# Kernel tuning notes

Hardware: AMD Instinct MI355X
Metric: run time of the kernel (lower is better)

The kernel has to match this reference:

```python
import jax, jax.numpy as jnp
import numpy as np

# Module dims (match init_kwargs): c_in=1, khop=3, f=128, c_out=2, f_out=128
N, KHOP, NNB, C_IN, F_IN = 2048, 3, 16, 1, 128
C_OUT, F_OUT = 2, 128
EPS_ROOT, EPS_NORM = 1e-8, 1e-7


def setup_inputs() -> dict:
    key = jax.random.key(0)
    k1, k2, k3 = jax.random.split(key, 3)
    x = jax.random.normal(k1, (N, C_IN, F_IN), jnp.float32)
    # dense form of the ragged neighbor[i][k] -> (n, c, f) lists
    neighbor = jax.random.normal(k2, (N, KHOP, NNB, C_IN, F_IN), jnp.float32)
    # Conv1d(khop*c_in, c_out*f_out, kernel_size=f, bias=False) weight
    W = jax.random.normal(k3, (C_OUT * F_OUT, KHOP * C_IN, F_IN), jnp.float32) * 0.05
    return {"x": x, "neighbor": neighbor, "W": W}


def _sgnroot(a):
    return jnp.sign(a) * jnp.sqrt(jnp.clip(jnp.abs(a), EPS_ROOT))


def _row_normalize(a):
    a = a / (jnp.abs(a).sum(-2, keepdims=True) + EPS_NORM)
    return jnp.where(jnp.isnan(a), 0.0, a)


def _feature_adjacency(x, neighbor):
    # x: (N,c,f), neighbor: (N,k,n,c,f) -> fadj: (N,k,f,f)
    fadj = jnp.einsum('Nca,Nkncb->Nkab', x, neighbor)
    fadj = fadj + jnp.swapaxes(fadj, -1, -2)
    return _row_normalize(_sgnroot(fadj))


def _transform(z, adj, W):
    # z: (..., c, f); adj: (..., K, f, f) broadcastable against z's batch dims
    # y[..., K, c, a] = sum_b adj[..., K, a, b] * z[..., c, b]
    y = jnp.einsum('...kab,...cb->...kca', adj, z)
    y = y.reshape(y.shape[:-3] + (KHOP * C_IN, F_IN))  # (..., k*c, f)
    # Conv1d with kernel_size == f and output length 1 == full contraction
    out = jnp.einsum('oqf,...qf->...o', W, y)
    return out.reshape(out.shape[:-1] + (C_OUT, F_OUT))


def reference(x, neighbor, W):
    adj = _feature_adjacency(x, neighbor)                     # (N,k,f,f)
    x_out = _transform(x, adj, W)                             # (N,c_out,f_out)
    # each neighbor[i,k] is transformed with the full per-sample adj[i]
    nbr_out = _transform(neighbor, adj[:, None, None], W)     # (N,k,n,c_out,f_out)
    return (x_out, nbr_out)
```

## Files before the change

kernel.cpp:

```cpp
#include <hip/hip_runtime.h>

typedef unsigned short u16;
typedef unsigned int u32;
typedef __bf16 bf16;
typedef __bf16 bf16x8 __attribute__((ext_vector_type(8)));
typedef __bf16 bf16x4 __attribute__((ext_vector_type(4)));
typedef float f32x4 __attribute__((ext_vector_type(4)));

#define NSAMP 2048
#define KH 3
#define NNBR 16
#define F 128
#define OUT_O 256
#define QT 384

#define ZLD 136
#define YLD 136

__device__ __forceinline__ bf16x4 cvt4(float4 v) {
    bf16x4 h;
    h[0] = (bf16)v.x; h[1] = (bf16)v.y; h[2] = (bf16)v.z; h[3] = (bf16)v.w;
    return h;
}

__global__ void wprep(const float* __restrict__ W, bf16* __restrict__ Wbf) {
    int i = blockIdx.x * 256 + threadIdx.x;
    if (i < OUT_O * QT) Wbf[i] = (bf16)W[i];
}

__launch_bounds__(512, 6)
__global__ void featkhop(const float* __restrict__ xg,
                         const float* __restrict__ ng,
                         const bf16* __restrict__ Wbf,
                         float* __restrict__ out) {
    __shared__ __align__(16) bf16 Zs[64 * ZLD];
    __shared__ __align__(16) bf16 Ys[2][64 * YLD];
    float* const xls = (float*)(Zs + 49 * ZLD);
    float* const sls = xls + F;
    float* const rsi = xls + 4 * F;

    const int i = blockIdx.x;
    const int t = threadIdx.x;
    const int lane = t & 63;
    const int w = t >> 6;
    const int lr = lane & 15;
    const int lg = lane >> 4;

    if (t < F / 4) {
        float4 v = *(const float4*)(xg + (size_t)i * F + t * 4);
        *(float4*)(xls + t * 4) = v;
        *(bf16x4*)(Zs + 0 * ZLD + t * 4) = cvt4(v);
    }
    const float* nb = ng + (size_t)i * (KH * NNBR * F);
    {
        #pragma unroll
        for (int c = 0; c < 3; ++c) {
            int j = c * 512 + t;
            float4 v = *(const float4*)(nb + j * 4);
            int fl = j * 4;
            int row = 1 + (fl >> 7);
            int b = fl & 127;
            *(bf16x4*)(Zs + row * ZLD + b) = cvt4(v);
        }
    }
    if (t < KH * F) {
        int q = t >> 7, b = t & 127;
        float s = 0.f;
        #pragma unroll
        for (int n = 0; n < NNBR; ++n) s += nb[(q * NNBR + n) * F + b];
        sls[q * F + b] = s;
    }
    __syncthreads();

    const int a_row = w * 16 + lr;
    const float x_a = xls[a_row];
    const int cbase = lg * 8;

    f32x4 acc2[4][2];
    {
        f32x4 zf = {0.f, 0.f, 0.f, 0.f};
        #pragma unroll
        for (int mt = 0; mt < 4; ++mt) { acc2[mt][0] = zf; acc2[mt][1] = zf; }
    }

    for (int q = 0; q < KH; ++q) {
        const float s_a = sls[q * F + a_row];
        bf16x8 uvh[4];
        float ps = 0.f;
        #pragma unroll
        for (int kk = 0; kk < 4; ++kk) {
            float4 xb0 = *(const float4*)(xls + kk * 32 + cbase);
            float4 xb1 = *(const float4*)(xls + kk * 32 + cbase + 4);
            float4 sb0 = *(const float4*)(sls + q * F + kk * 32 + cbase);
            float4 sb1 = *(const float4*)(sls + q * F + kk * 32 + cbase + 4);
            float xb[8] = {xb0.x, xb0.y, xb0.z, xb0.w, xb1.x, xb1.y, xb1.z, xb1.w};
            float sb[8] = {sb0.x, sb0.y, sb0.z, sb0.w, sb1.x, sb1.y, sb1.z, sb1.w};
            #pragma unroll
            for (int e = 0; e < 8; ++e) {
                float tv = x_a * sb[e] + xb[e] * s_a;
                float r = tv * __builtin_amdgcn_rsqf(fmaxf(fabsf(tv), 1e-8f));
                uvh[kk][e] = (bf16)r;
                ps += fabsf(r);
            }
        }
        ps += __shfl_xor(ps, 16);
        ps += __shfl_xor(ps, 32);
        if (lg == 0) rsi[a_row] = __builtin_amdgcn_rcpf(ps + 1e-7f);
        __syncthreads();

        bf16x8 afrag[4];
        #pragma unroll
        for (int kk = 0; kk < 4; ++kk) {
            float4 r0 = *(const float4*)(rsi + kk * 32 + cbase);
            float4 r1 = *(const float4*)(rsi + kk * 32 + cbase + 4);
            float rb[8] = {r0.x, r0.y, r0.z, r0.w, r1.x, r1.y, r1.z, r1.w};
            #pragma unroll
            for (int e = 0; e < 8; ++e)
                afrag[kk][e] = (bf16)((float)uvh[kk][e] * rb[e]);
        }

        bf16* Ysb = Ys[q & 1];
        #pragma unroll
        for (int mt = 0; mt < 4; ++mt) {
            f32x4 a1 = {0.f, 0.f, 0.f, 0.f};
            #pragma unroll
            for (int kk = 0; kk < 4; ++kk) {
                bf16x8 zfrag = *(const bf16x8*)(Zs + (mt * 16 + lr) * ZLD + kk * 32 + cbase);
                a1 = __builtin_amdgcn_mfma_f32_16x16x32_bf16(afrag[kk], zfrag, a1, 0, 0, 0);
            }
            bf16x4 yv;
            #pragma unroll
            for (int r = 0; r < 4; ++r) yv[r] = (bf16)a1[r];
            *(bf16x4*)(Ysb + (mt * 16 + lr) * YLD + w * 16 + lg * 4) = yv;
        }
        __syncthreads();

        #pragma unroll
        for (int kk = 0; kk < 4; ++kk) {
            const bf16* wp = Wbf + (size_t)(w * 32 + lr) * QT + q * F + kk * 32 + cbase;
            bf16x8 wf0 = *(const bf16x8*)wp;
            bf16x8 wf1 = *(const bf16x8*)(wp + 16 * QT);
            #pragma unroll
            for (int mt = 0; mt < 4; ++mt) {
                bf16x8 af = *(const bf16x8*)(Ysb + (mt * 16 + lr) * YLD + kk * 32 + cbase);
                acc2[mt][0] = __builtin_amdgcn_mfma_f32_16x16x32_bf16(af, wf0, acc2[mt][0], 0, 0, 0);
                acc2[mt][1] = __builtin_amdgcn_mfma_f32_16x16x32_bf16(af, wf1, acc2[mt][1], 0, 0, 0);
            }
        }
    }

    float* xout = out + (size_t)i * OUT_O;
    float* nout = out + (size_t)NSAMP * OUT_O + (size_t)i * 48 * OUT_O;
    #pragma unroll
    for (int mt = 0; mt < 4; ++mt) {
        #pragma unroll
        for (int r = 0; r < 4; ++r) {
            int v = mt * 16 + lg * 4 + r;
            #pragma unroll
            for (int nn = 0; nn < 2; ++nn) {
                int o = w * 32 + nn * 16 + lr;
                float val = acc2[mt][nn][r];
                if (v == 0) xout[o] = val;
                else if (v <= 48) nout[(size_t)(v - 1) * OUT_O + o] = val;
            }
        }
    }
}

extern "C" void kernel_launch(void* const* d_in, const int* in_sizes, int n_in,
                              void* d_out, int out_size, void* d_ws, size_t ws_size,
                              hipStream_t stream) {
    const float* x   = (const float*)d_in[0];
    const float* nbr = (const float*)d_in[1];
    const float* W   = (const float*)d_in[2];
    bf16* Wbf = (bf16*)d_ws;
    wprep<<<(OUT_O * QT + 255) / 256, 256, 0, stream>>>(W, Wbf);
    featkhop<<<NSAMP, 512, 0, stream>>>(x, nbr, Wbf, (float*)d_out);
}
```

Baseline: 95.85 us.

## Software-pipeline khop stages to cut barriers and overlap row build with GEMMs

Result: faster. 93.16 us (-2.8%).

```diff
diff --git a/kernel.cpp b/kernel.cpp
--- a/kernel.cpp
+++ b/kernel.cpp
@@ -28,16 +28,95 @@
     if (i < OUT_O * QT) Wbf[i] = (bf16)W[i];
 }
 
-__launch_bounds__(512, 6)
+
+__device__ __forceinline__ void build_row(int q, const float* xls, const float* sls,
+                                          float* rsb, bf16x8 uvh[4],
+                                          float x_a, int a_row, int cbase, int lg) {
+    const float s_a = sls[q * F + a_row];
+    float ps = 0.f;
+    #pragma unroll
+    for (int kk = 0; kk < 4; ++kk) {
+        float4 xb0 = *(const float4*)(xls + kk * 32 + cbase);
+        float4 xb1 = *(const float4*)(xls + kk * 32 + cbase + 4);
+        float4 sb0 = *(const float4*)(sls + q * F + kk * 32 + cbase);
+        float4 sb1 = *(const float4*)(sls + q * F + kk * 32 + cbase + 4);
+        float xb[8] = {xb0.x, xb0.y, xb0.z, xb0.w, xb1.x, xb1.y, xb1.z, xb1.w};
+        float sb[8] = {sb0.x, sb0.y, sb0.z, sb0.w, sb1.x, sb1.y, sb1.z, sb1.w};
+        #pragma unroll
+        for (int e = 0; e < 8; ++e) {
+            float tv = x_a * sb[e] + xb[e] * s_a;
+            float r = tv * __builtin_amdgcn_rsqf(fmaxf(fabsf(tv), 1e-8f));
+            uvh[kk][e] = (bf16)r;
+            ps += fabsf(r);
+        }
+    }
+    ps += __shfl_xor(ps, 16);
+    ps += __shfl_xor(ps, 32);
+    if (lg == 0) rsb[a_row] = __builtin_amdgcn_rcpf(ps + 1e-7f);
+}
+
+__device__ __forceinline__ void gemm1_store(const bf16x8 uvh[4], const float* rsb,
+                                            const bf16* Zs, bf16* Ysb,
+                                            int lr, int lg, int w, int cbase) {
+    bf16x8 afrag[4];
+    #pragma unroll
+    for (int kk = 0; kk < 4; ++kk) {
+        float4 r0 = *(const float4*)(rsb + kk * 32 + cbase);
+        float4 r1 = *(const float4*)(rsb + kk * 32 + cbase + 4);
+        float rb[8] = {r0.x, r0.y, r0.z, r0.w, r1.x, r1.y, r1.z, r1.w};
+        #pragma unroll
+        for (int e = 0; e < 8; ++e)
+            afrag[kk][e] = (bf16)((float)uvh[kk][e] * rb[e]);
+    }
+    f32x4 acc1[4];
+    {
+        f32x4 zf = {0.f, 0.f, 0.f, 0.f};
+        #pragma unroll
+        for (int mt = 0; mt < 4; ++mt) acc1[mt] = zf;
+    }
+    #pragma unroll
+    for (int kk = 0; kk < 4; ++kk) {
+        #pragma unroll
+        for (int mt = 0; mt < 4; ++mt) {
+            bf16x8 zfrag = *(const bf16x8*)(Zs + (mt * 16 + lr) * ZLD + kk * 32 + cbase);
+            acc1[mt] = __builtin_amdgcn_mfma_f32_16x16x32_bf16(afrag[kk], zfrag, acc1[mt], 0, 0, 0);
+        }
+    }
+    #pragma unroll
+    for (int mt = 0; mt < 4; ++mt) {
+        bf16x4 yv;
+        #pragma unroll
+        for (int r = 0; r < 4; ++r) yv[r] = (bf16)acc1[mt][r];
+        *(bf16x4*)(Ysb + (mt * 16 + lr) * YLD + w * 16 + lg * 4) = yv;
+    }
+}
+
+__device__ __forceinline__ void gemm2_acc(const bf16* Wq, const bf16* Ysb,
+                                          f32x4 acc2[4][2], int lr, int cbase) {
+    #pragma unroll
+    for (int kk = 0; kk < 4; ++kk) {
+        bf16x8 wf0 = *(const bf16x8*)(Wq + kk * 32 + cbase);
+        bf16x8 wf1 = *(const bf16x8*)(Wq + 16 * QT + kk * 32 + cbase);
+        #pragma unroll
+        for (int mt = 0; mt < 4; ++mt) {
+            bf16x8 af = *(const bf16x8*)(Ysb + (mt * 16 + lr) * YLD + kk * 32 + cbase);
+            acc2[mt][0] = __builtin_amdgcn_mfma_f32_16x16x32_bf16(af, wf0, acc2[mt][0], 0, 0, 0);
+            acc2[mt][1] = __builtin_amdgcn_mfma_f32_16x16x32_bf16(af, wf1, acc2[mt][1], 0, 0, 0);
+        }
+    }
+}
+
+__launch_bounds__(512, 4)
 __global__ void featkhop(const float* __restrict__ xg,
                          const float* __restrict__ ng,
                          const bf16* __restrict__ Wbf,
                          float* __restrict__ out) {
     __shared__ __align__(16) bf16 Zs[64 * ZLD];
     __shared__ __align__(16) bf16 Ys[2][64 * YLD];
-    float* const xls = (float*)(Zs + 49 * ZLD);
-    float* const sls = xls + F;
-    float* const rsi = xls + 4 * F;
+    float* const xls  = (float*)(Zs + 49 * ZLD);
+    float* const sls  = xls + F;
+    float* const rsi0 = xls + 4 * F;
+    float* const rsi1 = xls + 5 * F;
 
     const int i = blockIdx.x;
     const int t = threadIdx.x;
@@ -75,6 +154,7 @@
     const int a_row = w * 16 + lr;
     const float x_a = xls[a_row];
     const int cbase = lg * 8;
+    const bf16* Wbase = Wbf + (size_t)(w * 32 + lr) * QT;
 
     f32x4 acc2[4][2];
     {
@@ -83,71 +163,25 @@
         for (int mt = 0; mt < 4; ++mt) { acc2[mt][0] = zf; acc2[mt][1] = zf; }
     }
 
-    for (int q = 0; q < KH; ++q) {
-        const float s_a = sls[q * F + a_row];
-        bf16x8 uvh[4];
-        float ps = 0.f;
-        #pragma unroll
-        for (int kk = 0; kk < 4; ++kk) {
-            float4 xb0 = *(const float4*)(xls + kk * 32 + cbase);
-            float4 xb1 = *(const float4*)(xls + kk * 32 + cbase + 4);
-            float4 sb0 = *(const float4*)(sls + q * F + kk * 32 + cbase);
-            float4 sb1 = *(const float4*)(sls + q * F + kk * 32 + cbase + 4);
-            float xb[8] = {xb0.x, xb0.y, xb0.z, xb0.w, xb1.x, xb1.y, xb1.z, xb1.w};
-            float sb[8] = {sb0.x, sb0.y, sb0.z, sb0.w, sb1.x, sb1.y, sb1.z, sb1.w};
-            #pragma unroll
-            for (int e = 0; e < 8; ++e) {
-                float tv = x_a * sb[e] + xb[e] * s_a;
-                float r = tv * __builtin_amdgcn_rsqf(fmaxf(fabsf(tv), 1e-8f));
-                uvh[kk][e] = (bf16)r;
-                ps += fabsf(r);
-            }
-        }
-        ps += __shfl_xor(ps, 16);
-        ps += __shfl_xor(ps, 32);
-        if (lg == 0) rsi[a_row] = __builtin_amdgcn_rcpf(ps + 1e-7f);
-        __syncthreads();
-
-        bf16x8 afrag[4];
-        #pragma unroll
-        for (int kk = 0; kk < 4; ++kk) {
-            float4 r0 = *(const float4*)(rsi + kk * 32 + cbase);
-            float4 r1 = *(const float4*)(rsi + kk * 32 + cbase + 4);
-            float rb[8] = {r0.x, r0.y, r0.z, r0.w, r1.x, r1.y, r1.z, r1.w};
-            #pragma unroll
-            for (int e = 0; e < 8; ++e)
-                afrag[kk][e] = (bf16)((float)uvh[kk][e] * rb[e]);
-        }
-
-        bf16* Ysb = Ys[q & 1];
-        #pragma unroll
-        for (int mt = 0; mt < 4; ++mt) {
-            f32x4 a1 = {0.f, 0.f, 0.f, 0.f};
-            #pragma unroll
-            for (int kk = 0; kk < 4; ++kk) {
-                bf16x8 zfrag = *(const bf16x8*)(Zs + (mt * 16 + lr) * ZLD + kk * 32 + cbase);
-                a1 = __builtin_amdgcn_mfma_f32_16x16x32_bf16(afrag[kk], zfrag, a1, 0, 0, 0);
-            }
-            bf16x4 yv;
-            #pragma unroll
-            for (int r = 0; r < 4; ++r) yv[r] = (bf16)a1[r];
-            *(bf16x4*)(Ysb + (mt * 16 + lr) * YLD + w * 16 + lg * 4) = yv;
-        }
-        __syncthreads();
-
-        #pragma unroll
-        for (int kk = 0; kk < 4; ++kk) {
-            const bf16* wp = Wbf + (size_t)(w * 32 + lr) * QT + q * F + kk * 32 + cbase;
-            bf16x8 wf0 = *(const bf16x8*)wp;
-            bf16x8 wf1 = *(const bf16x8*)(wp + 16 * QT);
-            #pragma unroll
-            for (int mt = 0; mt < 4; ++mt) {
-                bf16x8 af = *(const bf16x8*)(Ysb + (mt * 16 + lr) * YLD + kk * 32 + cbase);
-                acc2[mt][0] = __builtin_amdgcn_mfma_f32_16x16x32_bf16(af, wf0, acc2[mt][0], 0, 0, 0);
-                acc2[mt][1] = __builtin_amdgcn_mfma_f32_16x16x32_bf16(af, wf1, acc2[mt][1], 0, 0, 0);
-            }
-        }
-    }
+    bf16x8 uvh[4];
+
+    build_row(0, xls, sls, rsi0, uvh, x_a, a_row, cbase, lg);
+    __syncthreads();
+
+    gemm1_store(uvh, rsi0, Zs, Ys[0], lr, lg, w, cbase);
+    build_row(1, xls, sls, rsi1, uvh, x_a, a_row, cbase, lg);
+    __syncthreads();
+
+    gemm2_acc(Wbase + 0 * F, Ys[0], acc2, lr, cbase);
+    gemm1_store(uvh, rsi1, Zs, Ys[1], lr, lg, w, cbase);
+    build_row(2, xls, sls, rsi0, uvh, x_a, a_row, cbase, lg);
+    __syncthreads();
+
+    gemm2_acc(Wbase + 1 * F, Ys[1], acc2, lr, cbase);
+    gemm1_store(uvh, rsi0, Zs, Ys[0], lr, lg, w, cbase);
+    __syncthreads();
+
+    gemm2_acc(Wbase + 2 * F, Ys[0], acc2, lr, cbase);
 
     float* xout = out + (size_t)i * OUT_O;
     float* nout = out + (size_t)NSAMP * OUT_O + (size_t)i * 48 * OUT_O;
```

## Double block to 1024 threads and split both GEMM stages across 16 waves

Applied to the files above, without the earlier changes.

Result: slower. 114.9 us (+19.9%).

```diff
diff --git a/kernel.cpp b/kernel.cpp
--- a/kernel.cpp
+++ b/kernel.cpp
@@ -28,13 +28,13 @@
     if (i < OUT_O * QT) Wbf[i] = (bf16)W[i];
 }
 
-__launch_bounds__(512, 6)
+__launch_bounds__(1024, 8)
 __global__ void featkhop(const float* __restrict__ xg,
                          const float* __restrict__ ng,
                          const bf16* __restrict__ Wbf,
                          float* __restrict__ out) {
     __shared__ __align__(16) bf16 Zs[64 * ZLD];
-    __shared__ __align__(16) bf16 Ys[2][64 * YLD];
+    __shared__ __align__(16) bf16 Ys[64 * YLD];
     float* const xls = (float*)(Zs + 49 * ZLD);
     float* const sls = xls + F;
     float* const rsi = xls + 4 * F;
@@ -43,6 +43,8 @@
     const int t = threadIdx.x;
     const int lane = t & 63;
     const int w = t >> 6;
+    const int wh = w & 7;
+    const int half = w >> 3;
     const int lr = lane & 15;
     const int lg = lane >> 4;
 
@@ -53,14 +55,17 @@
     }
     const float* nb = ng + (size_t)i * (KH * NNBR * F);
     {
-        #pragma unroll
-        for (int c = 0; c < 3; ++c) {
-            int j = c * 512 + t;
+        {
+            int j = t;
             float4 v = *(const float4*)(nb + j * 4);
             int fl = j * 4;
-            int row = 1 + (fl >> 7);
-            int b = fl & 127;
-            *(bf16x4*)(Zs + row * ZLD + b) = cvt4(v);
+            *(bf16x4*)(Zs + (1 + (fl >> 7)) * ZLD + (fl & 127)) = cvt4(v);
+        }
+        if (t < 512) {
+            int j = 1024 + t;
+            float4 v = *(const float4*)(nb + j * 4);
+            int fl = j * 4;
+            *(bf16x4*)(Zs + (1 + (fl >> 7)) * ZLD + (fl & 127)) = cvt4(v);
         }
     }
     if (t < KH * F) {
@@ -72,15 +77,15 @@
     }
     __syncthreads();
 
-    const int a_row = w * 16 + lr;
+    const int a_row = wh * 16 + lr;
     const float x_a = xls[a_row];
     const int cbase = lg * 8;
 
-    f32x4 acc2[4][2];
+    f32x4 acc2[4];
     {
         f32x4 zf = {0.f, 0.f, 0.f, 0.f};
         #pragma unroll
-        for (int mt = 0; mt < 4; ++mt) { acc2[mt][0] = zf; acc2[mt][1] = zf; }
+        for (int mt = 0; mt < 4; ++mt) acc2[mt] = zf;
     }
 
     for (int q = 0; q < KH; ++q) {
@@ -105,64 +110,56 @@
         }
         ps += __shfl_xor(ps, 16);
         ps += __shfl_xor(ps, 32);
-        if (lg == 0) rsi[a_row] = __builtin_amdgcn_rcpf(ps + 1e-7f);
+        if (lg == 0 && half == 0) rsi[a_row] = __builtin_amdgcn_rcpf(ps + 1e-7f);
         __syncthreads();
 
-        bf16x8 afrag[4];
+        f32x4 a10 = {0.f, 0.f, 0.f, 0.f};
+        f32x4 a11 = {0.f, 0.f, 0.f, 0.f};
         #pragma unroll
         for (int kk = 0; kk < 4; ++kk) {
             float4 r0 = *(const float4*)(rsi + kk * 32 + cbase);
             float4 r1 = *(const float4*)(rsi + kk * 32 + cbase + 4);
             float rb[8] = {r0.x, r0.y, r0.z, r0.w, r1.x, r1.y, r1.z, r1.w};
+            bf16x8 afrag;
             #pragma unroll
             for (int e = 0; e < 8; ++e)
-                afrag[kk][e] = (bf16)((float)uvh[kk][e] * rb[e]);
+                afrag[e] = (bf16)((float)uvh[kk][e] * rb[e]);
+            bf16x8 zf0 = *(const bf16x8*)(Zs + (half * 32 + lr) * ZLD + kk * 32 + cbase);
+            bf16x8 zf1 = *(const bf16x8*)(Zs + (half * 32 + 16 + lr) * ZLD + kk * 32 + cbase);
+            a10 = __builtin_amdgcn_mfma_f32_16x16x32_bf16(afrag, zf0, a10, 0, 0, 0);
+            a11 = __builtin_amdgcn_mfma_f32_16x16x32_bf16(afrag, zf1, a11, 0, 0, 0);
         }
-
-        bf16* Ysb = Ys[q & 1];
-        #pragma unroll
-        for (int mt = 0; mt < 4; ++mt) {
-            f32x4 a1 = {0.f, 0.f, 0.f, 0.f};
+        {
+            bf16x4 yv0, yv1;
             #pragma unroll
-            for (int kk = 0; kk < 4; ++kk) {
-                bf16x8 zfrag = *(const bf16x8*)(Zs + (mt * 16 + lr) * ZLD + kk * 32 + cbase);
-                a1 = __builtin_amdgcn_mfma_f32_16x16x32_bf16(afrag[kk], zfrag, a1, 0, 0, 0);
-            }
-            bf16x4 yv;
-            #pragma unroll
-            for (int r = 0; r < 4; ++r) yv[r] = (bf16)a1[r];
-            *(bf16x4*)(Ysb + (mt * 16 + lr) * YLD + w * 16 + lg * 4) = yv;
+            for (int r = 0; r < 4; ++r) { yv0[r] = (bf16)a10[r]; yv1[r] = (bf16)a11[r]; }
+            *(bf16x4*)(Ys + (half * 32 + lr) * YLD + wh * 16 + lg * 4) = yv0;
+            *(bf16x4*)(Ys + (half * 32 + 16 + lr) * YLD + wh * 16 + lg * 4) = yv1;
         }
         __syncthreads();
 
         #pragma unroll
         for (int kk = 0; kk < 4; ++kk) {
-            const bf16* wp = Wbf + (size_t)(w * 32 + lr) * QT + q * F + kk * 32 + cbase;
-            bf16x8 wf0 = *(const bf16x8*)wp;
-            bf16x8 wf1 = *(const bf16x8*)(wp + 16 * QT);
+            bf16x8 wf = *(const bf16x8*)(Wbf + (size_t)(w * 16 + lr) * QT + q * F + kk * 32 + cbase);
             #pragma unroll
             for (int mt = 0; mt < 4; ++mt) {
-                bf16x8 af = *(const bf16x8*)(Ysb + (mt * 16 + lr) * YLD + kk * 32 + cbase);
-                acc2[mt][0] = __builtin_amdgcn_mfma_f32_16x16x32_bf16(af, wf0, acc2[mt][0], 0, 0, 0);
-                acc2[mt][1] = __builtin_amdgcn_mfma_f32_16x16x32_bf16(af, wf1, acc2[mt][1], 0, 0, 0);
+                bf16x8 af = *(const bf16x8*)(Ys + (mt * 16 + lr) * YLD + kk * 32 + cbase);
+                acc2[mt] = __builtin_amdgcn_mfma_f32_16x16x32_bf16(af, wf, acc2[mt], 0, 0, 0);
             }
         }
     }
 
     float* xout = out + (size_t)i * OUT_O;
     float* nout = out + (size_t)NSAMP * OUT_O + (size_t)i * 48 * OUT_O;
+    const int o = w * 16 + lr;
     #pragma unroll
     for (int mt = 0; mt < 4; ++mt) {
         #pragma unroll
         for (int r = 0; r < 4; ++r) {
             int v = mt * 16 + lg * 4 + r;
-            #pragma unroll
-            for (int nn = 0; nn < 2; ++nn) {
-                int o = w * 32 + nn * 16 + lr;
-                float val = acc2[mt][nn][r];
-                if (v == 0) xout[o] = val;
-                else if (v <= 48) nout[(size_t)(v - 1) * OUT_O + o] = val;
-            }
+            float val = acc2[mt][r];
+            if (v == 0) xout[o] = val;
+            else if (v <= 48) nout[(size_t)(v - 1) * OUT_O + o] = val;
         }
     }
 }
@@ -175,5 +172,5 @@
     const float* W   = (const float*)d_in[2];
     bf16* Wbf = (bf16*)d_ws;
     wprep<<<(OUT_O * QT + 255) / 256, 256, 0, stream>>>(W, Wbf);
-    featkhop<<<NSAMP, 512, 0, stream>>>(x, nbr, Wbf, (float*)d_out);
+    featkhop<<<NSAMP, 1024, 0, stream>>>(x, nbr, Wbf, (float*)d_out);
 }
```
